# Kernel optimization log

Hardware: AMD Instinct MI355X
Metric: run time of the kernel (lower is better)

Reference implementation:

```python
import math
import jax, jax.numpy as jnp
import numpy as np

TILE = 128
CAUSAL = True


def setup_inputs() -> dict:
    key = jax.random.key(0)
    kq, kk, kv = jax.random.split(key, 3)
    B, H, T, D = 2, 16, 4096, 64
    query = jax.random.normal(kq, (B, H, T, D), dtype=jnp.float32)
    k = jax.random.normal(kk, (B, H, T, D), dtype=jnp.float32)
    v = jax.random.normal(kv, (B, H, T, D), dtype=jnp.float32)
    return {"query": query, "key": k, "value": v}


def flash_attention(q, k, v, causal=CAUSAL, tile=TILE):
    B, H, T, D = q.shape
    nt = T // tile
    scale = 1.0 / math.sqrt(D)
    # (nt, B, H, tile, D) stacks of key/value tiles
    k_tiles = jnp.moveaxis(k.reshape(B, H, nt, tile, D), 2, 0)
    v_tiles = jnp.moveaxis(v.reshape(B, H, nt, tile, D), 2, 0)
    k_idx_tiles = jnp.arange(T, dtype=jnp.int32).reshape(nt, tile)
    q_idx = jnp.arange(T, dtype=jnp.int32)  # (T,)

    m0 = jnp.full((B, H, T), -jnp.inf, dtype=q.dtype)
    s0 = jnp.zeros((B, H, T), dtype=q.dtype)
    acc0 = jnp.zeros((B, H, T, D), dtype=q.dtype)

    def step(carry, inp):
        m, s, acc = carry
        k_t, v_t, k_idx = inp
        # scores: (B, H, T, tile)
        scores = jnp.einsum('bhqd,bhkd->bhqk', q, k_t) * scale
        if causal:
            mask = k_idx[None, None, None, :] > q_idx[None, None, :, None]
            scores = jnp.where(mask, -jnp.inf, scores)
        tile_max = scores.max(axis=-1)                       # (B,H,T)
        new_m = jnp.maximum(m, tile_max)
        alpha = jnp.exp(m - new_m)                           # (B,H,T)
        p = jnp.exp(scores - new_m[..., None])               # (B,H,T,tile)
        s = s * alpha + p.sum(axis=-1)
        acc = acc * alpha[..., None] + jnp.einsum('bhqk,bhkd->bhqd', p, v_t)
        return (new_m, s, acc), None

    (m, s, acc), _ = jax.lax.scan(step, (m0, s0, acc0), (k_tiles, v_tiles, k_idx_tiles))
    return acc / s[..., None]


def reference(query, key, value):
    return flash_attention(query, key, value)
```

## Files before the change

kernel.cpp:

```cpp
#include <hip/hip_runtime.h>

#define T_SEQ 4096
#define DIM   64
#define NQT   32
#define QTILE 128
#define KTILE 128
#define NBH   32
#define NCHUNK_TOT 80

typedef __attribute__((ext_vector_type(8)))  short bhalf8;
typedef __attribute__((ext_vector_type(16))) float floatx16;

#if __has_builtin(__builtin_amdgcn_exp2f)
#define EXP2F(x) __builtin_amdgcn_exp2f(x)
#else
#define EXP2F(x) exp2f(x)
#endif

__device__ __forceinline__ int sig23(int s) {
  return (s & ~12) | ((s & 4) << 1) | ((s & 8) >> 1);
}

__device__ __forceinline__ unsigned pk2bf(float a, float b) {
  unsigned ua = __builtin_bit_cast(unsigned, a) + 0x8000u;
  unsigned ub = __builtin_bit_cast(unsigned, b) + 0x8000u;
  return __builtin_amdgcn_perm(ub, ua, 0x07060302u);
}

__device__ __forceinline__ float bflo(unsigned u) {
  return __builtin_bit_cast(float, u << 16);
}
__device__ __forceinline__ float bfhi(unsigned u) {
  return __builtin_bit_cast(float, u & 0xffff0000u);
}

union FragU { unsigned u[4]; bhalf8 v; };

__device__ __forceinline__ void gload_lds16(const void* g, void* l) {
#if __has_builtin(__builtin_amdgcn_global_load_lds)
  __builtin_amdgcn_global_load_lds(
      (const __attribute__((address_space(1))) unsigned*)g,
      (__attribute__((address_space(3))) unsigned*)l, 16, 0, 0);
#else
  *(uint4*)l = *(const uint4*)g;
#endif
}

__global__ __launch_bounds__(256, 2) void fa_prep(
    const float* __restrict__ K, const float* __restrict__ V,
    unsigned short* __restrict__ Kb, unsigned short* __restrict__ Vb) {
  const int tid = threadIdx.x;
  const int bid = blockIdx.x;
  const int bh = bid >> 5, kt = bid & 31;
  __shared__ __align__(16) unsigned short SS[16384];
  __shared__ __align__(16) float VS[128 * 68];
  unsigned short* Kl = SS;
  unsigned short* Vt = SS + 8192;
  const int base = bh * (T_SEQ * DIM) + kt * (KTILE * DIM);

  {
    const float4* kp4 = reinterpret_cast<const float4*>(K + base);
    float4 kx[8];
#pragma unroll
    for (int c = 0; c < 8; ++c) kx[c] = kp4[tid + 256 * c];
#pragma unroll
    for (int c = 0; c < 8; ++c) {
      int f4 = tid + 256 * c;
      int kv = f4 >> 4;
      int d0 = (f4 & 15) << 2;
      unsigned lo = pk2bf(kx[c].x, kx[c].y);
      unsigned hi = pk2bf(kx[c].z, kx[c].w);
      unsigned long long u64 = (unsigned long long)lo | ((unsigned long long)hi << 32);
      int idx = (kv << 6) | ((((d0 >> 3) ^ (kv & 7)) << 3) | (d0 & 7));
      *reinterpret_cast<unsigned long long*>(&Kl[idx]) = u64;
    }
  }
  {
    const float4* vp4 = reinterpret_cast<const float4*>(V + base);
#pragma unroll
    for (int c = 0; c < 8; ++c) {
      float4 x = vp4[tid + 256 * c];
      int f4 = tid + 256 * c;
      int kv = f4 >> 4;
      int d0 = (f4 & 15) << 2;
      *reinterpret_cast<float4*>(&VS[kv * 68 + d0]) = x;
    }
  }
  __syncthreads();
  {
    const int s0 = (tid & 63) << 1;
    const int db = (tid >> 6) << 4;
    const int kva = sig23(s0);
    const int kvb = kva + 1;
    float4 va[4], vb[4];
#pragma unroll
    for (int sg = 0; sg < 4; ++sg) {
      va[sg] = *reinterpret_cast<const float4*>(&VS[kva * 68 + db + 4 * sg]);
      vb[sg] = *reinterpret_cast<const float4*>(&VS[kvb * 68 + db + 4 * sg]);
    }
    const float* vaf = reinterpret_cast<const float*>(va);
    const float* vbf = reinterpret_cast<const float*>(vb);
#pragma unroll
    for (int j = 0; j < 16; ++j) {
      int d = db + j;
      unsigned u = pk2bf(vaf[j], vbf[j]);
      int idx = (d << 7) | ((((s0 >> 3) ^ (d & 15)) << 3) | (s0 & 7));
      *reinterpret_cast<unsigned*>(&Vt[idx]) = u;
    }
  }
  __syncthreads();
  const uint4* S4 = reinterpret_cast<const uint4*>(SS);
  uint4* KbT = reinterpret_cast<uint4*>(Kb + (size_t)(bh * 32 + kt) * 8192);
  uint4* VbT = reinterpret_cast<uint4*>(Vb + (size_t)(bh * 32 + kt) * 8192);
#pragma unroll
  for (int i = 0; i < 4; ++i) KbT[tid + 256 * i] = S4[tid + 256 * i];
#pragma unroll
  for (int i = 0; i < 4; ++i) VbT[tid + 256 * i] = S4[1024 + tid + 256 * i];
}

__global__ __launch_bounds__(256, 2) void fa_main(
    const float* __restrict__ Q, const unsigned short* __restrict__ Kb,
    const unsigned short* __restrict__ Vb,
    unsigned short* __restrict__ Op, float* __restrict__ ML) {
  const int tid  = threadIdx.x;
  const int w    = tid >> 6;
  const int lane = tid & 63;
  const int n    = lane & 31;
  const int h    = lane >> 5;
  const int bid  = blockIdx.x;
  const int bh   = bid & (NBH - 1);
  const int f    = (NCHUNK_TOT - 1) - (bid >> 5);

  int qt, ch;
  if (f < 8)       { qt = f;                         ch = 0; }
  else if (f < 24) { int g = f - 8;  qt = 8  + (g >> 1); ch = g & 1; }
  else if (f < 48) { int g = f - 24; int q3 = g / 3; qt = 16 + q3; ch = g - 3 * q3; }
  else             { int g = f - 48; qt = 24 + (g >> 2); ch = g & 3; }

  const int k0   = ch * 8;
  const int kend = min(k0 + 8, qt + 1);
  const int base = bh * (T_SEQ * DIM);

  __shared__ __align__(16) unsigned short Kl[KTILE * DIM];
  __shared__ __align__(16) unsigned short Vt[DIM * KTILE];

  const int qrow = qt * QTILE + w * 32 + n;
  const float cs = 0.125f * 1.44269504088896340736f;
  FragU qf[4];
  {
    const float* qp = Q + base + qrow * DIM + h * 8;
#pragma unroll
    for (int ks = 0; ks < 4; ++ks) {
      float4 a = *reinterpret_cast<const float4*>(qp + 16 * ks);
      float4 b = *reinterpret_cast<const float4*>(qp + 16 * ks + 4);
      qf[ks].u[0] = pk2bf(a.x * cs, a.y * cs);
      qf[ks].u[1] = pk2bf(a.z * cs, a.w * cs);
      qf[ks].u[2] = pk2bf(b.x * cs, b.y * cs);
      qf[ks].u[3] = pk2bf(b.z * cs, b.w * cs);
    }
  }

  floatx16 o0, o1;
#pragma unroll
  for (int i = 0; i < 16; ++i) { o0[i] = 0.f; o1[i] = 0.f; }
  float s_run = 0.f;

  const int soff = w * 4096 + lane * 16;

  for (int kt = k0; kt < kend; ++kt) {
    __syncthreads();
    {
      const char* kb = reinterpret_cast<const char*>(Kb) + (size_t)((bh << 5) + kt) * 16384;
      const char* vb = reinterpret_cast<const char*>(Vb) + (size_t)((bh << 5) + kt) * 16384;
      char* kl = reinterpret_cast<char*>(Kl);
      char* vl = reinterpret_cast<char*>(Vt);
#pragma unroll
      for (int r = 0; r < 4; ++r)
        gload_lds16(kb + soff + r * 1024, kl + soff + r * 1024);
#pragma unroll
      for (int r = 0; r < 4; ++r)
        gload_lds16(vb + soff + r * 1024, vl + soff + r * 1024);
    }
    __syncthreads();

    floatx16 st[4];
#pragma unroll
    for (int tt = 0; tt < 4; ++tt) {
      floatx16 acc;
#pragma unroll
      for (int i = 0; i < 16; ++i) acc[i] = 0.f;
#pragma unroll
      for (int ks = 0; ks < 4; ++ks) {
        const bhalf8 kfrag = *reinterpret_cast<const bhalf8*>(
            &Kl[((32 * tt + n) << 6) | (((2 * ks + h) ^ (n & 7)) << 3)]);
        acc = __builtin_amdgcn_mfma_f32_32x32x16_bf16(kfrag, qf[ks].v, acc, 0, 0, 0);
      }
      st[tt] = acc;
    }

    if (kt == qt) {
#pragma unroll
      for (int tt = 0; tt < 4; ++tt)
#pragma unroll
        for (int r = 0; r < 16; ++r) {
          int kvloc = 32 * tt + (r & 3) + 8 * (r >> 2) + 4 * h;
          st[tt][r] = (kvloc > 32 * w + n) ? -__builtin_inff() : st[tt][r];
        }
    }

    float psum = 0.f;
#pragma unroll
    for (int tt = 0; tt < 4; ++tt)
#pragma unroll
      for (int r = 0; r < 16; ++r) {
        float p = EXP2F(st[tt][r]);
        st[tt][r] = p;
        psum += p;
      }
    psum += __shfl_xor(psum, 32, 64);
    s_run += psum;

#pragma unroll
    for (int tt = 0; tt < 4; ++tt) {
      FragU b0, b1;
      b0.u[0] = pk2bf(st[tt][0],  st[tt][1]);
      b0.u[1] = pk2bf(st[tt][2],  st[tt][3]);
      b0.u[2] = pk2bf(st[tt][4],  st[tt][5]);
      b0.u[3] = pk2bf(st[tt][6],  st[tt][7]);
      b1.u[0] = pk2bf(st[tt][8],  st[tt][9]);
      b1.u[1] = pk2bf(st[tt][10], st[tt][11]);
      b1.u[2] = pk2bf(st[tt][12], st[tt][13]);
      b1.u[3] = pk2bf(st[tt][14], st[tt][15]);

      const int sw = n & 15;
      const bhalf8 v00 = *reinterpret_cast<const bhalf8*>(
          &Vt[(n << 7) | (((4 * tt + 0 + h) ^ sw) << 3)]);
      const bhalf8 v01 = *reinterpret_cast<const bhalf8*>(
          &Vt[(n << 7) | (((4 * tt + 2 + h) ^ sw) << 3)]);
      const bhalf8 v10 = *reinterpret_cast<const bhalf8*>(
          &Vt[((32 + n) << 7) | (((4 * tt + 0 + h) ^ sw) << 3)]);
      const bhalf8 v11 = *reinterpret_cast<const bhalf8*>(
          &Vt[((32 + n) << 7) | (((4 * tt + 2 + h) ^ sw) << 3)]);
      o0 = __builtin_amdgcn_mfma_f32_32x32x16_bf16(v00, b0.v, o0, 0, 0, 0);
      o0 = __builtin_amdgcn_mfma_f32_32x32x16_bf16(v01, b1.v, o0, 0, 0, 0);
      o1 = __builtin_amdgcn_mfma_f32_32x32x16_bf16(v10, b0.v, o1, 0, 0, 0);
      o1 = __builtin_amdgcn_mfma_f32_32x32x16_bf16(v11, b1.v, o1, 0, 0, 0);
    }
  }

  const int pidx = (((bh << 5) | qt) << 2) | ch;
  unsigned* opr = reinterpret_cast<unsigned*>(Op) + (size_t)pidx * 4096 + (w * 32 + n) * 32;
#pragma unroll
  for (int g = 0; g < 4; ++g) {
    opr[4 * g + 2 * h]          = pk2bf(o0[4 * g],     o0[4 * g + 1]);
    opr[4 * g + 2 * h + 1]      = pk2bf(o0[4 * g + 2], o0[4 * g + 3]);
    opr[16 + 4 * g + 2 * h]     = pk2bf(o1[4 * g],     o1[4 * g + 1]);
    opr[16 + 4 * g + 2 * h + 1] = pk2bf(o1[4 * g + 2], o1[4 * g + 3]);
  }
  if (h == 0) ML[(pidx << 7) + w * 32 + n] = s_run;
}

__global__ __launch_bounds__(256, 2) void fa_combine(
    const unsigned short* __restrict__ Op, const float* __restrict__ ML,
    float* __restrict__ O) {
  const int bid = blockIdx.x;
  const int bh = bid >> 5, qt = bid & 31;
  const int nch = (qt >> 3) + 1;
  const int t = threadIdx.x;
  const int r = t >> 1, half = t & 1;
  const int pbase = ((bh << 5) | qt) << 2;

  float L = 0.f;
  for (int i = 0; i < nch; ++i) L += ML[((pbase + i) << 7) + r];

  float acc[32];
#pragma unroll
  for (int j = 0; j < 32; ++j) acc[j] = 0.f;

  for (int i = 0; i < nch; ++i) {
    const uint4* p = reinterpret_cast<const uint4*>(
        Op + (size_t)(pbase + i) * 8192 + r * 64 + 32 * half);
    uint4 q4[4];
#pragma unroll
    for (int j = 0; j < 4; ++j) q4[j] = p[j];
    const unsigned* u = reinterpret_cast<const unsigned*>(q4);
#pragma unroll
    for (int j = 0; j < 16; ++j) {
      acc[2 * j]     += bflo(u[j]);
      acc[2 * j + 1] += bfhi(u[j]);
    }
  }
  const float inv = 1.0f / L;
  float* op = O + (size_t)bh * (T_SEQ * DIM) + (size_t)(qt * 128 + r) * DIM + 32 * half;
#pragma unroll
  for (int g = 0; g < 8; ++g) {
    float4 x;
    x.x = acc[4 * g] * inv;  x.y = acc[4 * g + 1] * inv;
    x.z = acc[4 * g + 2] * inv;  x.w = acc[4 * g + 3] * inv;
    *reinterpret_cast<float4*>(op + 4 * g) = x;
  }
}

__global__ __launch_bounds__(256, 2) void fa_mono(
    const float* __restrict__ Q, const float* __restrict__ K,
    const float* __restrict__ V, float* __restrict__ O) {
  const int tid  = threadIdx.x;
  const int w    = tid >> 6;
  const int lane = tid & 63;
  const int n    = lane & 31;
  const int h    = lane >> 5;
  const int bid  = blockIdx.x;
  const int bh   = bid & (NBH - 1);
  const int qt   = (NQT - 1) - (bid >> 5);

  const int base = bh * (T_SEQ * DIM);
  __shared__ __align__(16) unsigned short Kl[KTILE * DIM];
  __shared__ __align__(16) unsigned short Vt[DIM * KTILE];

  const int qrow = qt * QTILE + w * 32 + n;
  const float cs = 0.125f * 1.44269504088896340736f;
  FragU qf[4];
  {
    const float* qp = Q + base + qrow * DIM + h * 8;
#pragma unroll
    for (int ks = 0; ks < 4; ++ks) {
      float4 a = *reinterpret_cast<const float4*>(qp + 16 * ks);
      float4 b = *reinterpret_cast<const float4*>(qp + 16 * ks + 4);
      qf[ks].u[0] = pk2bf(a.x * cs, a.y * cs);
      qf[ks].u[1] = pk2bf(a.z * cs, a.w * cs);
      qf[ks].u[2] = pk2bf(b.x * cs, b.y * cs);
      qf[ks].u[3] = pk2bf(b.z * cs, b.w * cs);
    }
  }

  floatx16 o0, o1;
#pragma unroll
  for (int i = 0; i < 16; ++i) { o0[i] = 0.f; o1[i] = 0.f; }
  float s_run = 0.f;

  for (int kt = 0; kt <= qt; ++kt) {
    __syncthreads();
    {
      const float4* kp4 = reinterpret_cast<const float4*>(K + base + kt * (KTILE * DIM));
      float4 kx[8];
#pragma unroll
      for (int c = 0; c < 8; ++c) kx[c] = kp4[tid + 256 * c];
#pragma unroll
      for (int c = 0; c < 8; ++c) {
        int f4 = tid + 256 * c;
        int kv = f4 >> 4;
        int d0 = (f4 & 15) << 2;
        unsigned lo = pk2bf(kx[c].x, kx[c].y);
        unsigned hi = pk2bf(kx[c].z, kx[c].w);
        unsigned long long u64 = (unsigned long long)lo | ((unsigned long long)hi << 32);
        int idx = (kv << 6) | ((((d0 >> 3) ^ (kv & 7)) << 3) | (d0 & 7));
        *reinterpret_cast<unsigned long long*>(&Kl[idx]) = u64;
      }
      const int s0 = (tid & 63) << 1;
      const int db = (tid >> 6) << 4;
      const int kva = sig23(s0);
      const float* vr0 = V + base + kt * (KTILE * DIM) + kva * DIM + db;
      const float* vr1 = vr0 + DIM;
      float4 va[4], vb[4];
#pragma unroll
      for (int sg = 0; sg < 4; ++sg) {
        va[sg] = *reinterpret_cast<const float4*>(vr0 + 4 * sg);
        vb[sg] = *reinterpret_cast<const float4*>(vr1 + 4 * sg);
      }
      const float* vaf = reinterpret_cast<const float*>(va);
      const float* vbf = reinterpret_cast<const float*>(vb);
#pragma unroll
      for (int j = 0; j < 16; ++j) {
        int d = db + j;
        unsigned u = pk2bf(vaf[j], vbf[j]);
        int idx = (d << 7) | ((((s0 >> 3) ^ (d & 15)) << 3) | (s0 & 7));
        *reinterpret_cast<unsigned*>(&Vt[idx]) = u;
      }
    }
    __syncthreads();

    floatx16 st[4];
#pragma unroll
    for (int tt = 0; tt < 4; ++tt) {
      floatx16 acc;
#pragma unroll
      for (int i = 0; i < 16; ++i) acc[i] = 0.f;
#pragma unroll
      for (int ks = 0; ks < 4; ++ks) {
        const bhalf8 kfrag = *reinterpret_cast<const bhalf8*>(
            &Kl[((32 * tt + n) << 6) | (((2 * ks + h) ^ (n & 7)) << 3)]);
        acc = __builtin_amdgcn_mfma_f32_32x32x16_bf16(kfrag, qf[ks].v, acc, 0, 0, 0);
      }
      st[tt] = acc;
    }

    if (kt == qt) {
#pragma unroll
      for (int tt = 0; tt < 4; ++tt)
#pragma unroll
        for (int r = 0; r < 16; ++r) {
          int kvloc = 32 * tt + (r & 3) + 8 * (r >> 2) + 4 * h;
          st[tt][r] = (kvloc > 32 * w + n) ? -__builtin_inff() : st[tt][r];
        }
    }

    float psum = 0.f;
#pragma unroll
    for (int tt = 0; tt < 4; ++tt)
#pragma unroll
      for (int r = 0; r < 16; ++r) {
        float p = EXP2F(st[tt][r]);
        st[tt][r] = p;
        psum += p;
      }
    psum += __shfl_xor(psum, 32, 64);
    s_run += psum;

#pragma unroll
    for (int tt = 0; tt < 4; ++tt) {
      FragU b0, b1;
      b0.u[0] = pk2bf(st[tt][0],  st[tt][1]);
      b0.u[1] = pk2bf(st[tt][2],  st[tt][3]);
      b0.u[2] = pk2bf(st[tt][4],  st[tt][5]);
      b0.u[3] = pk2bf(st[tt][6],  st[tt][7]);
      b1.u[0] = pk2bf(st[tt][8],  st[tt][9]);
      b1.u[1] = pk2bf(st[tt][10], st[tt][11]);
      b1.u[2] = pk2bf(st[tt][12], st[tt][13]);
      b1.u[3] = pk2bf(st[tt][14], st[tt][15]);

      const int sw = n & 15;
      const bhalf8 v00 = *reinterpret_cast<const bhalf8*>(
          &Vt[(n << 7) | (((4 * tt + 0 + h) ^ sw) << 3)]);
      const bhalf8 v01 = *reinterpret_cast<const bhalf8*>(
          &Vt[(n << 7) | (((4 * tt + 2 + h) ^ sw) << 3)]);
      const bhalf8 v10 = *reinterpret_cast<const bhalf8*>(
          &Vt[((32 + n) << 7) | (((4 * tt + 0 + h) ^ sw) << 3)]);
      const bhalf8 v11 = *reinterpret_cast<const bhalf8*>(
          &Vt[((32 + n) << 7) | (((4 * tt + 2 + h) ^ sw) << 3)]);
      o0 = __builtin_amdgcn_mfma_f32_32x32x16_bf16(v00, b0.v, o0, 0, 0, 0);
      o0 = __builtin_amdgcn_mfma_f32_32x32x16_bf16(v01, b1.v, o0, 0, 0, 0);
      o1 = __builtin_amdgcn_mfma_f32_32x32x16_bf16(v10, b0.v, o1, 0, 0, 0);
      o1 = __builtin_amdgcn_mfma_f32_32x32x16_bf16(v11, b1.v, o1, 0, 0, 0);
    }
  }

  const float inv = 1.0f / s_run;
  float* op = O + base + qrow * DIM;
#pragma unroll
  for (int g = 0; g < 4; ++g) {
    float4 x, y;
    x.x = o0[4 * g] * inv;  x.y = o0[4 * g + 1] * inv;
    x.z = o0[4 * g + 2] * inv;  x.w = o0[4 * g + 3] * inv;
    y.x = o1[4 * g] * inv;  y.y = o1[4 * g + 1] * inv;
    y.z = o1[4 * g + 2] * inv;  y.w = o1[4 * g + 3] * inv;
    *reinterpret_cast<float4*>(op + 8 * g + 4 * h)      = x;
    *reinterpret_cast<float4*>(op + 32 + 8 * g + 4 * h) = y;
  }
}

extern "C" void kernel_launch(void* const* d_in, const int* in_sizes, int n_in,
                              void* d_out, int out_size, void* d_ws, size_t ws_size,
                              hipStream_t stream) {
  (void)in_sizes; (void)n_in; (void)out_size;
  const float* Q = (const float*)d_in[0];
  const float* K = (const float*)d_in[1];
  const float* V = (const float*)d_in[2];
  float* O = (float*)d_out;

  const size_t OFF_KB = 0;
  const size_t OFF_VB = 16777216;
  const size_t OFF_OP = 33554432;
  const size_t OFF_ML = 100663296;
  const size_t NEED   = 102760448;

  if (ws_size >= NEED) {
    unsigned short* Kb = (unsigned short*)((char*)d_ws + OFF_KB);
    unsigned short* Vb = (unsigned short*)((char*)d_ws + OFF_VB);
    unsigned short* Op = (unsigned short*)((char*)d_ws + OFF_OP);
    float*          ML = (float*)((char*)d_ws + OFF_ML);
    fa_prep<<<dim3(NBH * NQT), dim3(256), 0, stream>>>(K, V, Kb, Vb);
    fa_main<<<dim3(NBH * NCHUNK_TOT), dim3(256), 0, stream>>>(Q, Kb, Vb, Op, ML);
    fa_combine<<<dim3(NBH * NQT), dim3(256), 0, stream>>>(Op, ML, O);
  } else {
    fa_mono<<<dim3(NQT * NBH), dim3(256), 0, stream>>>(Q, K, V, O);
  }
}
```

Measured before the change: 232.9 us.

## Shrink KV tiles to 64 rows and raise main-kernel occupancy

The prep kernel now writes bf16 K and V in 64-row sub-tiles with matching swizzles. The main kernel loads 64-key tiles, so LDS use per block drops to 16 KB, which lets launch bounds rise from 2 to 4 blocks per CU. It also interleaves exp, packing and PV MFMA per 32-key slice instead of materialising all scores, which lowers register pressure. Packing to bf16 switches to the hardware cvt_pk intrinsic where it is available. The cost is twice as many loop iterations and barriers for the same work.

```diff
diff --git a/kernel.cpp b/kernel.cpp
--- a/kernel.cpp
+++ b/kernel.cpp
@@ -4,7 +4,6 @@
 #define DIM   64
 #define NQT   32
 #define QTILE 128
-#define KTILE 128
 #define NBH   32
 #define NCHUNK_TOT 80
 
@@ -26,6 +25,14 @@
   unsigned ub = __builtin_bit_cast(unsigned, b) + 0x8000u;
   return __builtin_amdgcn_perm(ub, ua, 0x07060302u);
 }
+#if __has_builtin(__builtin_amdgcn_cvt_pk_bf16_f32)
+typedef __attribute__((ext_vector_type(2))) __bf16 bf16x2_t;
+__device__ __forceinline__ unsigned cvtpk(float a, float b) {
+  return __builtin_bit_cast(unsigned, __builtin_amdgcn_cvt_pk_bf16_f32(a, b));
+}
+#else
+__device__ __forceinline__ unsigned cvtpk(float a, float b) { return pk2bf(a, b); }
+#endif
 
 __device__ __forceinline__ float bflo(unsigned u) {
   return __builtin_bit_cast(float, u << 16);
@@ -54,9 +61,7 @@
   const int bh = bid >> 5, kt = bid & 31;
   __shared__ __align__(16) unsigned short SS[16384];
   __shared__ __align__(16) float VS[128 * 68];
-  unsigned short* Kl = SS;
-  unsigned short* Vt = SS + 8192;
-  const int base = bh * (T_SEQ * DIM) + kt * (KTILE * DIM);
+  const int base = bh * (T_SEQ * DIM) + kt * (128 * DIM);
 
   {
     const float4* kp4 = reinterpret_cast<const float4*>(K + base);
@@ -71,8 +76,9 @@
       unsigned lo = pk2bf(kx[c].x, kx[c].y);
       unsigned hi = pk2bf(kx[c].z, kx[c].w);
       unsigned long long u64 = (unsigned long long)lo | ((unsigned long long)hi << 32);
-      int idx = (kv << 6) | ((((d0 >> 3) ^ (kv & 7)) << 3) | (d0 & 7));
-      *reinterpret_cast<unsigned long long*>(&Kl[idx]) = u64;
+      int jt = kv >> 6, kvl = kv & 63;
+      int idx = jt * 4096 + (kvl << 6) + ((((d0 >> 3) ^ (kvl & 7)) << 3) | (d0 & 7));
+      *reinterpret_cast<unsigned long long*>(&SS[idx]) = u64;
     }
   }
   {
@@ -90,7 +96,8 @@
   {
     const int s0 = (tid & 63) << 1;
     const int db = (tid >> 6) << 4;
-    const int kva = sig23(s0);
+    const int jt = s0 >> 6, sl = s0 & 63;
+    const int kva = jt * 64 + sig23(sl);
     const int kvb = kva + 1;
     float4 va[4], vb[4];
 #pragma unroll
@@ -104,8 +111,8 @@
     for (int j = 0; j < 16; ++j) {
       int d = db + j;
       unsigned u = pk2bf(vaf[j], vbf[j]);
-      int idx = (d << 7) | ((((s0 >> 3) ^ (d & 15)) << 3) | (s0 & 7));
-      *reinterpret_cast<unsigned*>(&Vt[idx]) = u;
+      int idx = 8192 + jt * 4096 + (d << 6) + ((((sl >> 3) ^ (d & 7)) << 3) | (sl & 7));
+      *reinterpret_cast<unsigned*>(&SS[idx]) = u;
     }
   }
   __syncthreads();
@@ -118,7 +125,7 @@
   for (int i = 0; i < 4; ++i) VbT[tid + 256 * i] = S4[1024 + tid + 256 * i];
 }
 
-__global__ __launch_bounds__(256, 2) void fa_main(
+__global__ __launch_bounds__(256, 4) void fa_main(
     const float* __restrict__ Q, const unsigned short* __restrict__ Kb,
     const unsigned short* __restrict__ Vb,
     unsigned short* __restrict__ Op, float* __restrict__ ML) {
@@ -137,12 +144,180 @@
   else if (f < 48) { int g = f - 24; int q3 = g / 3; qt = 16 + q3; ch = g - 3 * q3; }
   else             { int g = f - 48; qt = 24 + (g >> 2); ch = g & 3; }
 
-  const int k0   = ch * 8;
-  const int kend = min(k0 + 8, qt + 1);
+  const int k0   = ch << 4;
+  const int kend = min(k0 + 16, 2 * qt + 2);
   const int base = bh * (T_SEQ * DIM);
 
-  __shared__ __align__(16) unsigned short Kl[KTILE * DIM];
-  __shared__ __align__(16) unsigned short Vt[DIM * KTILE];
+  __shared__ __align__(16) unsigned short Kl[4096];
+  __shared__ __align__(16) unsigned short Vt[4096];
+
+  const int qrow = qt * QTILE + w * 32 + n;
+  const float cs = 0.125f * 1.44269504088896340736f;
+  FragU qf[4];
+  {
+    const float* qp = Q + base + qrow * DIM + h * 8;
+#pragma unroll
+    for (int ks = 0; ks < 4; ++ks) {
+      float4 a = *reinterpret_cast<const float4*>(qp + 16 * ks);
+      float4 b = *reinterpret_cast<const float4*>(qp + 16 * ks + 4);
+      qf[ks].u[0] = cvtpk(a.x * cs, a.y * cs);
+      qf[ks].u[1] = cvtpk(a.z * cs, a.w * cs);
+      qf[ks].u[2] = cvtpk(b.x * cs, b.y * cs);
+      qf[ks].u[3] = cvtpk(b.z * cs, b.w * cs);
+    }
+  }
+
+  floatx16 o0, o1, zc;
+#pragma unroll
+  for (int i = 0; i < 16; ++i) { o0[i] = 0.f; o1[i] = 0.f; zc[i] = 0.f; }
+  float s_run = 0.f;
+
+  const int soff = w * 2048 + lane * 16;
+  const char* kb0 = reinterpret_cast<const char*>(Kb) + (size_t)(bh * 64) * 8192;
+  const char* vb0 = reinterpret_cast<const char*>(Vb) + (size_t)(bh * 64) * 8192;
+
+  for (int kt = k0; kt < kend; ++kt) {
+    __syncthreads();
+    {
+      const char* kb = kb0 + (size_t)kt * 8192;
+      const char* vb = vb0 + (size_t)kt * 8192;
+      char* kl = reinterpret_cast<char*>(Kl);
+      char* vl = reinterpret_cast<char*>(Vt);
+      gload_lds16(kb + soff,        kl + soff);
+      gload_lds16(kb + soff + 1024, kl + soff + 1024);
+      gload_lds16(vb + soff,        vl + soff);
+      gload_lds16(vb + soff + 1024, vl + soff + 1024);
+    }
+    __syncthreads();
+
+    float psum = 0.f;
+#pragma unroll
+    for (int tt = 0; tt < 2; ++tt) {
+      floatx16 st;
+      {
+        const bhalf8 k0f = *reinterpret_cast<const bhalf8*>(
+            &Kl[((32 * tt + n) << 6) | (((0 + h) ^ (n & 7)) << 3)]);
+        st = __builtin_amdgcn_mfma_f32_32x32x16_bf16(k0f, qf[0].v, zc, 0, 0, 0);
+#pragma unroll
+        for (int ks = 1; ks < 4; ++ks) {
+          const bhalf8 kfr = *reinterpret_cast<const bhalf8*>(
+              &Kl[((32 * tt + n) << 6) | (((2 * ks + h) ^ (n & 7)) << 3)]);
+          st = __builtin_amdgcn_mfma_f32_32x32x16_bf16(kfr, qf[ks].v, st, 0, 0, 0);
+        }
+      }
+
+      if (kt >= 2 * qt) {
+        const int lim = (w << 5) + n - ((kt - 2 * qt) << 6);
+#pragma unroll
+        for (int r = 0; r < 16; ++r) {
+          int kvl = 32 * tt + (r & 3) + 8 * (r >> 2) + 4 * h;
+          st[r] = (kvl > lim) ? -__builtin_inff() : st[r];
+        }
+      }
+
+#pragma unroll
+      for (int r = 0; r < 16; ++r) {
+        float p = EXP2F(st[r]);
+        st[r] = p;
+        psum += p;
+      }
+
+      FragU b0, b1;
+      b0.u[0] = cvtpk(st[0],  st[1]);
+      b0.u[1] = cvtpk(st[2],  st[3]);
+      b0.u[2] = cvtpk(st[4],  st[5]);
+      b0.u[3] = cvtpk(st[6],  st[7]);
+      b1.u[0] = cvtpk(st[8],  st[9]);
+      b1.u[1] = cvtpk(st[10], st[11]);
+      b1.u[2] = cvtpk(st[12], st[13]);
+      b1.u[3] = cvtpk(st[14], st[15]);
+
+      const int sw = n & 7;
+      const bhalf8 v00 = *reinterpret_cast<const bhalf8*>(
+          &Vt[(n << 6) | (((4 * tt + 0 + h) ^ sw) << 3)]);
+      const bhalf8 v01 = *reinterpret_cast<const bhalf8*>(
+          &Vt[(n << 6) | (((4 * tt + 2 + h) ^ sw) << 3)]);
+      const bhalf8 v10 = *reinterpret_cast<const bhalf8*>(
+          &Vt[((32 + n) << 6) | (((4 * tt + 0 + h) ^ sw) << 3)]);
+      const bhalf8 v11 = *reinterpret_cast<const bhalf8*>(
+          &Vt[((32 + n) << 6) | (((4 * tt + 2 + h) ^ sw) << 3)]);
+      o0 = __builtin_amdgcn_mfma_f32_32x32x16_bf16(v00, b0.v, o0, 0, 0, 0);
+      o0 = __builtin_amdgcn_mfma_f32_32x32x16_bf16(v01, b1.v, o0, 0, 0, 0);
+      o1 = __builtin_amdgcn_mfma_f32_32x32x16_bf16(v10, b0.v, o1, 0, 0, 0);
+      o1 = __builtin_amdgcn_mfma_f32_32x32x16_bf16(v11, b1.v, o1, 0, 0, 0);
+    }
+    psum += __shfl_xor(psum, 32, 64);
+    s_run += psum;
+  }
+
+  const int pidx = (((bh << 5) | qt) << 2) | ch;
+  unsigned* opr = reinterpret_cast<unsigned*>(Op) + (size_t)pidx * 4096 + (w * 32 + n) * 32;
+#pragma unroll
+  for (int g = 0; g < 4; ++g) {
+    opr[4 * g + 2 * h]          = cvtpk(o0[4 * g],     o0[4 * g + 1]);
+    opr[4 * g + 2 * h + 1]      = cvtpk(o0[4 * g + 2], o0[4 * g + 3]);
+    opr[16 + 4 * g + 2 * h]     = cvtpk(o1[4 * g],     o1[4 * g + 1]);
+    opr[16 + 4 * g + 2 * h + 1] = cvtpk(o1[4 * g + 2], o1[4 * g + 3]);
+  }
+  if (h == 0) ML[(pidx << 7) + w * 32 + n] = s_run;
+}
+
+__global__ __launch_bounds__(256, 2) void fa_combine(
+    const unsigned short* __restrict__ Op, const float* __restrict__ ML,
+    float* __restrict__ O) {
+  const int bid = blockIdx.x;
+  const int bh = bid >> 5, qt = bid & 31;
+  const int nch = (qt >> 3) + 1;
+  const int t = threadIdx.x;
+  const int r = t >> 1, half = t & 1;
+  const int pbase = ((bh << 5) | qt) << 2;
+
+  float L = 0.f;
+  for (int i = 0; i < nch; ++i) L += ML[((pbase + i) << 7) + r];
+
+  float acc[32];
+#pragma unroll
+  for (int j = 0; j < 32; ++j) acc[j] = 0.f;
+
+  for (int i = 0; i < nch; ++i) {
+    const uint4* p = reinterpret_cast<const uint4*>(
+        Op + (size_t)(pbase + i) * 8192 + r * 64 + 32 * half);
+    uint4 q4[4];
+#pragma unroll
+    for (int j = 0; j < 4; ++j) q4[j] = p[j];
+    const unsigned* u = reinterpret_cast<const unsigned*>(q4);
+#pragma unroll
+    for (int j = 0; j < 16; ++j) {
+      acc[2 * j]     += bflo(u[j]);
+      acc[2 * j + 1] += bfhi(u[j]);
+    }
+  }
+  const float inv = 1.0f / L;
+  float* op = O + (size_t)bh * (T_SEQ * DIM) + (size_t)(qt * 128 + r) * DIM + 32 * half;
+#pragma unroll
+  for (int g = 0; g < 8; ++g) {
+    float4 x;
+    x.x = acc[4 * g] * inv;  x.y = acc[4 * g + 1] * inv;
+    x.z = acc[4 * g + 2] * inv;  x.w = acc[4 * g + 3] * inv;
+    *reinterpret_cast<float4*>(op + 4 * g) = x;
+  }
+}
+
+__global__ __launch_bounds__(256, 2) void fa_mono(
+    const float* __restrict__ Q, const float* __restrict__ K,
+    const float* __restrict__ V, float* __restrict__ O) {
+  const int tid  = threadIdx.x;
+  const int w    = tid >> 6;
+  const int lane = tid & 63;
+  const int n    = lane & 31;
+  const int h    = lane >> 5;
+  const int bid  = blockIdx.x;
+  const int bh   = bid & (NBH - 1);
+  const int qt   = (NQT - 1) - (bid >> 5);
+
+  const int base = bh * (T_SEQ * DIM);
+  __shared__ __align__(16) unsigned short Kl[128 * DIM];
+  __shared__ __align__(16) unsigned short Vt[DIM * 128];
 
   const int qrow = qt * QTILE + w * 32 + n;
   const float cs = 0.125f * 1.44269504088896340736f;
@@ -165,21 +340,44 @@
   for (int i = 0; i < 16; ++i) { o0[i] = 0.f; o1[i] = 0.f; }
   float s_run = 0.f;
 
-  const int soff = w * 4096 + lane * 16;
-
-  for (int kt = k0; kt < kend; ++kt) {
+  for (int kt = 0; kt <= qt; ++kt) {
     __syncthreads();
     {
-      const char* kb = reinterpret_cast<const char*>(Kb) + (size_t)((bh << 5) + kt) * 16384;
-      const char* vb = reinterpret_cast<const char*>(Vb) + (size_t)((bh << 5) + kt) * 16384;
-      char* kl = reinterpret_cast<char*>(Kl);
-      char* vl = reinterpret_cast<char*>(Vt);
-#pragma unroll
-      for (int r = 0; r < 4; ++r)
-        gload_lds16(kb + soff + r * 1024, kl + soff + r * 1024);
-#pragma unroll
-      for (int r = 0; r < 4; ++r)
-        gload_lds16(vb + soff + r * 1024, vl + soff + r * 1024);
+      const float4* kp4 = reinterpret_cast<const float4*>(K + base + kt * (128 * DIM));
+      float4 kx[8];
+#pragma unroll
+      for (int c = 0; c < 8; ++c) kx[c] = kp4[tid + 256 * c];
+#pragma unroll
+      for (int c = 0; c < 8; ++c) {
+        int f4 = tid + 256 * c;
+        int kv = f4 >> 4;
+        int d0 = (f4 & 15) << 2;
+        unsigned lo = pk2bf(kx[c].x, kx[c].y);
+        unsigned hi = pk2bf(kx[c].z, kx[c].w);
+        unsigned long long u64 = (unsigned long long)lo | ((unsigned long long)hi << 32);
+        int idx = (kv << 6) | ((((d0 >> 3) ^ (kv & 7)) << 3) | (d0 & 7));
+        *reinterpret_cast<unsigned long long*>(&Kl[idx]) = u64;
+      }
+      const int s0 = (tid & 63) << 1;
+      const int db = (tid >> 6) << 4;
+      const int kva = sig23(s0);
+      const float* vr0 = V + base + kt * (128 * DIM) + kva * DIM + db;
+      const float* vr1 = vr0 + DIM;
+      float4 va[4], vb[4];
+#pragma unroll
+      for (int sg = 0; sg < 4; ++sg) {
+        va[sg] = *reinterpret_cast<const float4*>(vr0 + 4 * sg);
+        vb[sg] = *reinterpret_cast<const float4*>(vr1 + 4 * sg);
+      }
+      const float* vaf = reinterpret_cast<const float*>(va);
+      const float* vbf = reinterpret_cast<const float*>(vb);
+#pragma unroll
+      for (int j = 0; j < 16; ++j) {
+        int d = db + j;
+        unsigned u = pk2bf(vaf[j], vbf[j]);
+        int idx = (d << 7) | ((((s0 >> 3) ^ (d & 15)) << 3) | (s0 & 7));
+        *reinterpret_cast<unsigned*>(&Vt[idx]) = u;
+      }
     }
     __syncthreads();
 
@@ -248,202 +446,6 @@
     }
   }
 
-  const int pidx = (((bh << 5) | qt) << 2) | ch;
-  unsigned* opr = reinterpret_cast<unsigned*>(Op) + (size_t)pidx * 4096 + (w * 32 + n) * 32;
-#pragma unroll
-  for (int g = 0; g < 4; ++g) {
-    opr[4 * g + 2 * h]          = pk2bf(o0[4 * g],     o0[4 * g + 1]);
-    opr[4 * g + 2 * h + 1]      = pk2bf(o0[4 * g + 2], o0[4 * g + 3]);
-    opr[16 + 4 * g + 2 * h]     = pk2bf(o1[4 * g],     o1[4 * g + 1]);
-    opr[16 + 4 * g + 2 * h + 1] = pk2bf(o1[4 * g + 2], o1[4 * g + 3]);
-  }
-  if (h == 0) ML[(pidx << 7) + w * 32 + n] = s_run;
-}
-
-__global__ __launch_bounds__(256, 2) void fa_combine(
-    const unsigned short* __restrict__ Op, const float* __restrict__ ML,
-    float* __restrict__ O) {
-  const int bid = blockIdx.x;
-  const int bh = bid >> 5, qt = bid & 31;
-  const int nch = (qt >> 3) + 1;
-  const int t = threadIdx.x;
-  const int r = t >> 1, half = t & 1;
-  const int pbase = ((bh << 5) | qt) << 2;
-
-  float L = 0.f;
-  for (int i = 0; i < nch; ++i) L += ML[((pbase + i) << 7) + r];
-
-  float acc[32];
-#pragma unroll
-  for (int j = 0; j < 32; ++j) acc[j] = 0.f;
-
-  for (int i = 0; i < nch; ++i) {
-    const uint4* p = reinterpret_cast<const uint4*>(
-        Op + (size_t)(pbase + i) * 8192 + r * 64 + 32 * half);
-    uint4 q4[4];
-#pragma unroll
-    for (int j = 0; j < 4; ++j) q4[j] = p[j];
-    const unsigned* u = reinterpret_cast<const unsigned*>(q4);
-#pragma unroll
-    for (int j = 0; j < 16; ++j) {
-      acc[2 * j]     += bflo(u[j]);
-      acc[2 * j + 1] += bfhi(u[j]);
-    }
-  }
-  const float inv = 1.0f / L;
-  float* op = O + (size_t)bh * (T_SEQ * DIM) + (size_t)(qt * 128 + r) * DIM + 32 * half;
-#pragma unroll
-  for (int g = 0; g < 8; ++g) {
-    float4 x;
-    x.x = acc[4 * g] * inv;  x.y = acc[4 * g + 1] * inv;
-    x.z = acc[4 * g + 2] * inv;  x.w = acc[4 * g + 3] * inv;
-    *reinterpret_cast<float4*>(op + 4 * g) = x;
-  }
-}
-
-__global__ __launch_bounds__(256, 2) void fa_mono(
-    const float* __restrict__ Q, const float* __restrict__ K,
-    const float* __restrict__ V, float* __restrict__ O) {
-  const int tid  = threadIdx.x;
-  const int w    = tid >> 6;
-  const int lane = tid & 63;
-  const int n    = lane & 31;
-  const int h    = lane >> 5;
-  const int bid  = blockIdx.x;
-  const int bh   = bid & (NBH - 1);
-  const int qt   = (NQT - 1) - (bid >> 5);
-
-  const int base = bh * (T_SEQ * DIM);
-  __shared__ __align__(16) unsigned short Kl[KTILE * DIM];
-  __shared__ __align__(16) unsigned short Vt[DIM * KTILE];
-
-  const int qrow = qt * QTILE + w * 32 + n;
-  const float cs = 0.125f * 1.44269504088896340736f;
-  FragU qf[4];
-  {
-    const float* qp = Q + base + qrow * DIM + h * 8;
-#pragma unroll
-    for (int ks = 0; ks < 4; ++ks) {
-      float4 a = *reinterpret_cast<const float4*>(qp + 16 * ks);
-      float4 b = *reinterpret_cast<const float4*>(qp + 16 * ks + 4);
-      qf[ks].u[0] = pk2bf(a.x * cs, a.y * cs);
-      qf[ks].u[1] = pk2bf(a.z * cs, a.w * cs);
-      qf[ks].u[2] = pk2bf(b.x * cs, b.y * cs);
-      qf[ks].u[3] = pk2bf(b.z * cs, b.w * cs);
-    }
-  }
-
-  floatx16 o0, o1;
-#pragma unroll
-  for (int i = 0; i < 16; ++i) { o0[i] = 0.f; o1[i] = 0.f; }
-  float s_run = 0.f;
-
-  for (int kt = 0; kt <= qt; ++kt) {
-    __syncthreads();
-    {
-      const float4* kp4 = reinterpret_cast<const float4*>(K + base + kt * (KTILE * DIM));
-      float4 kx[8];
-#pragma unroll
-      for (int c = 0; c < 8; ++c) kx[c] = kp4[tid + 256 * c];
-#pragma unroll
-      for (int c = 0; c < 8; ++c) {
-        int f4 = tid + 256 * c;
-        int kv = f4 >> 4;
-        int d0 = (f4 & 15) << 2;
-        unsigned lo = pk2bf(kx[c].x, kx[c].y);
-        unsigned hi = pk2bf(kx[c].z, kx[c].w);
-        unsigned long long u64 = (unsigned long long)lo | ((unsigned long long)hi << 32);
-        int idx = (kv << 6) | ((((d0 >> 3) ^ (kv & 7)) << 3) | (d0 & 7));
-        *reinterpret_cast<unsigned long long*>(&Kl[idx]) = u64;
-      }
-      const int s0 = (tid & 63) << 1;
-      const int db = (tid >> 6) << 4;
-      const int kva = sig23(s0);
-      const float* vr0 = V + base + kt * (KTILE * DIM) + kva * DIM + db;
-      const float* vr1 = vr0 + DIM;
-      float4 va[4], vb[4];
-#pragma unroll
-      for (int sg = 0; sg < 4; ++sg) {
-        va[sg] = *reinterpret_cast<const float4*>(vr0 + 4 * sg);
-        vb[sg] = *reinterpret_cast<const float4*>(vr1 + 4 * sg);
-      }
-      const float* vaf = reinterpret_cast<const float*>(va);
-      const float* vbf = reinterpret_cast<const float*>(vb);
-#pragma unroll
-      for (int j = 0; j < 16; ++j) {
-        int d = db + j;
-        unsigned u = pk2bf(vaf[j], vbf[j]);
-        int idx = (d << 7) | ((((s0 >> 3) ^ (d & 15)) << 3) | (s0 & 7));
-        *reinterpret_cast<unsigned*>(&Vt[idx]) = u;
-      }
-    }
-    __syncthreads();
-
-    floatx16 st[4];
-#pragma unroll
-    for (int tt = 0; tt < 4; ++tt) {
-      floatx16 acc;
-#pragma unroll
-      for (int i = 0; i < 16; ++i) acc[i] = 0.f;
-#pragma unroll
-      for (int ks = 0; ks < 4; ++ks) {
-        const bhalf8 kfrag = *reinterpret_cast<const bhalf8*>(
-            &Kl[((32 * tt + n) << 6) | (((2 * ks + h) ^ (n & 7)) << 3)]);
-        acc = __builtin_amdgcn_mfma_f32_32x32x16_bf16(kfrag, qf[ks].v, acc, 0, 0, 0);
-      }
-      st[tt] = acc;
-    }
-
-    if (kt == qt) {
-#pragma unroll
-      for (int tt = 0; tt < 4; ++tt)
-#pragma unroll
-        for (int r = 0; r < 16; ++r) {
-          int kvloc = 32 * tt + (r & 3) + 8 * (r >> 2) + 4 * h;
-          st[tt][r] = (kvloc > 32 * w + n) ? -__builtin_inff() : st[tt][r];
-        }
-    }
-
-    float psum = 0.f;
-#pragma unroll
-    for (int tt = 0; tt < 4; ++tt)
-#pragma unroll
-      for (int r = 0; r < 16; ++r) {
-        float p = EXP2F(st[tt][r]);
-        st[tt][r] = p;
-        psum += p;
-      }
-    psum += __shfl_xor(psum, 32, 64);
-    s_run += psum;
-
-#pragma unroll
-    for (int tt = 0; tt < 4; ++tt) {
-      FragU b0, b1;
-      b0.u[0] = pk2bf(st[tt][0],  st[tt][1]);
-      b0.u[1] = pk2bf(st[tt][2],  st[tt][3]);
-      b0.u[2] = pk2bf(st[tt][4],  st[tt][5]);
-      b0.u[3] = pk2bf(st[tt][6],  st[tt][7]);
-      b1.u[0] = pk2bf(st[tt][8],  st[tt][9]);
-      b1.u[1] = pk2bf(st[tt][10], st[tt][11]);
-      b1.u[2] = pk2bf(st[tt][12], st[tt][13]);
-      b1.u[3] = pk2bf(st[tt][14], st[tt][15]);
-
-      const int sw = n & 15;
-      const bhalf8 v00 = *reinterpret_cast<const bhalf8*>(
-          &Vt[(n << 7) | (((4 * tt + 0 + h) ^ sw) << 3)]);
-      const bhalf8 v01 = *reinterpret_cast<const bhalf8*>(
-          &Vt[(n << 7) | (((4 * tt + 2 + h) ^ sw) << 3)]);
-      const bhalf8 v10 = *reinterpret_cast<const bhalf8*>(
-          &Vt[((32 + n) << 7) | (((4 * tt + 0 + h) ^ sw) << 3)]);
-      const bhalf8 v11 = *reinterpret_cast<const bhalf8*>(
-          &Vt[((32 + n) << 7) | (((4 * tt + 2 + h) ^ sw) << 3)]);
-      o0 = __builtin_amdgcn_mfma_f32_32x32x16_bf16(v00, b0.v, o0, 0, 0, 0);
-      o0 = __builtin_amdgcn_mfma_f32_32x32x16_bf16(v01, b1.v, o0, 0, 0, 0);
-      o1 = __builtin_amdgcn_mfma_f32_32x32x16_bf16(v10, b0.v, o1, 0, 0, 0);
-      o1 = __builtin_amdgcn_mfma_f32_32x32x16_bf16(v11, b1.v, o1, 0, 0, 0);
-    }
-  }
-
   const float inv = 1.0f / s_run;
   float* op = O + base + qrow * DIM;
 #pragma unroll
```

Result: no change. 236.2 us (+1.4%).
